# Kernel optimization log

Hardware: AMD Instinct MI355X
Metric: run time of the kernel (lower is better)

Reference implementation:

```python
import jax, jax.numpy as jnp
import numpy as np

DIM = 512
NUM_HEADS = 8
HEAD_DIM = DIM // NUM_HEADS
SCALE = HEAD_DIM ** -0.5


def setup_inputs() -> dict:
    key = jax.random.key(0)
    ks = jax.random.split(key, 11)
    B, T, D = 2, 4096, DIM
    s = 0.02
    return {
        "query": jax.random.normal(ks[0], (B, T, D), jnp.float32),
        "key_": jax.random.normal(ks[1], (B, T, D), jnp.float32),
        "value": jax.random.normal(ks[2], (B, T, D), jnp.float32),
        "Wq": jax.random.normal(ks[3], (D, D), jnp.float32) * s,
        "bq": jnp.zeros((D,), jnp.float32),
        "Wk": jax.random.normal(ks[4], (D, D), jnp.float32) * s,
        "bk": jnp.zeros((D,), jnp.float32),
        "Wv": jax.random.normal(ks[5], (D, D), jnp.float32) * s,
        "bv": jnp.zeros((D,), jnp.float32),
        "Wo": jax.random.normal(ks[6], (D, D), jnp.float32) * s,
        "bo": jnp.zeros((D,), jnp.float32),
    }


def reference(query, key_, value, Wq, bq, Wk, bk, Wv, bv, Wo, bo):
    B, T, D = query.shape
    H, Hd = NUM_HEADS, HEAD_DIM
    # Linear projections (torch Linear: x @ W.T + b)
    q = (query @ Wq.T + bq).reshape(B, T, H, Hd).transpose(0, 2, 1, 3)   # [B,H,T,Hd]
    k = (key_ @ Wk.T + bk).reshape(B, -1, H, Hd).transpose(0, 2, 1, 3)    # [B,H,S,Hd]
    v = (value @ Wv.T + bv).reshape(B, -1, H, Hd).transpose(0, 2, 1, 3)   # [B,H,S,Hd]
    # Full O(T*S) score matrix, as in the original (non-fused) module
    scores = jnp.einsum("bhtd,bhsd->bhts", q, k) * SCALE                  # [B,H,T,S]
    weights = jax.nn.softmax(scores, axis=-1)
    out = jnp.einsum("bhts,bhsd->bhtd", weights, v)                       # [B,H,T,Hd]
    out = out.transpose(0, 2, 1, 3).reshape(B, T, D)
    return out @ Wo.T + bo
```

## Files before the change

### kernel.cpp

```cpp
#include <hip/hip_runtime.h>
#include <cstdint>
#include <cstddef>

typedef __attribute__((ext_vector_type(8))) __bf16 bf16x8;
typedef __attribute__((ext_vector_type(4))) float  f32x4;
typedef __attribute__((ext_vector_type(8))) unsigned short us8;

#define MFMA(a, b, c) __builtin_amdgcn_mfma_f32_16x16x32_bf16((a), (b), (c), 0, 0, 0)

#define QSCALE 0.18033688011112042f

__device__ __forceinline__ unsigned short f2bf(float f) {
  unsigned u = __float_as_uint(f);
  u += 0x7fffu + ((u >> 16) & 1u);
  return (unsigned short)(u >> 16);
}

__device__ __forceinline__ void gload16(const void* g, void* l) {
  __builtin_amdgcn_global_load_lds(
      (__attribute__((address_space(1))) unsigned int*)(uintptr_t)g,
      (__attribute__((address_space(3))) unsigned int*)l,
      16, 0, 0);
}

struct CastArgs {
  const float*    src[7];
  unsigned short* dst[7];
  int             n4[7];
};
__global__ __launch_bounds__(256) void cast_kernel(CastArgs a) {
  int z = blockIdx.y;
  const float* __restrict__ in = a.src[z];
  unsigned short* __restrict__ out = a.dst[z];
  int i = blockIdx.x * 256 + threadIdx.x;
  if (i < a.n4[z]) {
    float4 f = ((const float4*)in)[i];
    ushort4 r;
    r.x = f2bf(f.x); r.y = f2bf(f.y); r.z = f2bf(f.z); r.w = f2bf(f.w);
    ((ushort4*)out)[i] = r;
  }
}

struct ProjArgs {
  const unsigned short* X[3];
  const unsigned short* W[3];
  const float*          bias[3];
  unsigned short*       out[3];
};

__global__ __launch_bounds__(256) void proj_qkv_kernel(ProjArgs args) {
  __shared__ alignas(16) unsigned short smem[64 * 136];
  unsigned short* sA = smem;
  unsigned short* sB = smem + 4096;

  const int z = blockIdx.z;
  const unsigned short* __restrict__ X   = args.X[z];
  const unsigned short* __restrict__ W   = args.W[z];
  const float* __restrict__ bias         = args.bias[z];
  unsigned short* __restrict__ out       = args.out[z];
  const float scl = (z == 0) ? QSCALE : 1.0f;

  const int t = threadIdx.x;
  const int w = t >> 6, lane = t & 63;
  const int quad = lane >> 4, l15 = lane & 15;
  const int wr = w >> 1, wc = w & 1;
  const int m0 = blockIdx.x * 128, n0 = blockIdx.y * 128;

  const int srow = t >> 2;
  const int scol = (((t & 3) ^ (srow & 3)) << 3);

  f32x4 acc[4][4] = {};

  for (int k0 = 0; k0 < 512; k0 += 32) {
    __syncthreads();
    gload16(X + (size_t)(m0 + srow) * 512 + k0 + scol,      &sA[w * 512]);
    gload16(X + (size_t)(m0 + srow + 64) * 512 + k0 + scol, &sA[2048 + w * 512]);
    gload16(W + (size_t)(n0 + srow) * 512 + k0 + scol,      &sB[w * 512]);
    gload16(W + (size_t)(n0 + srow + 64) * 512 + k0 + scol, &sB[2048 + w * 512]);
    asm volatile("s_waitcnt vmcnt(0)" ::: "memory");
    __syncthreads();

    bf16x8 af[4], bfr[4];
#pragma unroll
    for (int mt = 0; mt < 4; ++mt) {
      int ra = wr * 64 + mt * 16 + l15;
      af[mt] = *(const bf16x8*)&sA[ra * 32 + ((quad ^ (ra & 3)) << 3)];
    }
#pragma unroll
    for (int nt = 0; nt < 4; ++nt) {
      int rb = wc * 64 + nt * 16 + l15;
      bfr[nt] = *(const bf16x8*)&sB[rb * 32 + ((quad ^ (rb & 3)) << 3)];
    }
#pragma unroll
    for (int mt = 0; mt < 4; ++mt)
#pragma unroll
      for (int nt = 0; nt < 4; ++nt)
        acc[mt][nt] = MFMA(af[mt], bfr[nt], acc[mt][nt]);
  }

  if (z != 2) {
#pragma unroll
    for (int nt = 0; nt < 4; ++nt) {
      int n = n0 + wc * 64 + nt * 16 + l15;
      float bv = bias[n];
      int h = n >> 6, hd = n & 63;
#pragma unroll
      for (int mt = 0; mt < 4; ++mt) {
#pragma unroll
        for (int r = 0; r < 4; ++r) {
          int m = m0 + wr * 64 + mt * 16 + quad * 4 + r;
          int b = m >> 12, tt = m & 4095;
          out[(((size_t)(b * 8 + h)) * 4096 + tt) * 64 + hd] =
              f2bf((acc[mt][nt][r] + bv) * scl);
        }
      }
    }
  } else {
    const int b   = m0 >> 12;
    const int tt0 = m0 & 4095;
#pragma unroll
    for (int h2 = 0; h2 < 2; ++h2) {
      __syncthreads();
      if (wc == h2) {
#pragma unroll
        for (int nt = 0; nt < 4; ++nt) {
          int nl = nt * 16 + l15;
          float bv = bias[n0 + h2 * 64 + nl];
#pragma unroll
          for (int mt = 0; mt < 4; ++mt)
#pragma unroll
            for (int r = 0; r < 4; ++r) {
              int ml = wr * 64 + mt * 16 + quad * 4 + r;
              smem[nl * 136 + ml] = f2bf((acc[mt][nt][r] + bv) * scl);
            }
        }
      }
      __syncthreads();
      const int row = t >> 2;
      const int c4  = (t & 3) * 8;
      const int n   = n0 + h2 * 64 + row;
      unsigned short* dst = out + ((size_t)(b * 512 + n)) * 4096 + tt0;
#pragma unroll
      for (int k = 0; k < 4; ++k)
        *(us8*)(dst + c4 + k * 32) = *(const us8*)&smem[row * 136 + c4 + k * 32];
    }
  }
}

__global__ __launch_bounds__(256) void proj_out_kernel(
    const unsigned short* __restrict__ X, const unsigned short* __restrict__ W,
    const float* __restrict__ bias, float* __restrict__ out) {
  __shared__ alignas(16) unsigned short sA[128 * 32];
  __shared__ alignas(16) unsigned short sB[128 * 32];

  const int t = threadIdx.x;
  const int w = t >> 6, lane = t & 63;
  const int quad = lane >> 4, l15 = lane & 15;
  const int wr = w >> 1, wc = w & 1;
  const int m0 = blockIdx.x * 128, n0 = blockIdx.y * 128;
  const int srow = t >> 2;
  const int scol = (((t & 3) ^ (srow & 3)) << 3);

  f32x4 acc[4][4] = {};

  for (int k0 = 0; k0 < 512; k0 += 32) {
    __syncthreads();
    gload16(X + (size_t)(m0 + srow) * 512 + k0 + scol,      &sA[w * 512]);
    gload16(X + (size_t)(m0 + srow + 64) * 512 + k0 + scol, &sA[2048 + w * 512]);
    gload16(W + (size_t)(n0 + srow) * 512 + k0 + scol,      &sB[w * 512]);
    gload16(W + (size_t)(n0 + srow + 64) * 512 + k0 + scol, &sB[2048 + w * 512]);
    asm volatile("s_waitcnt vmcnt(0)" ::: "memory");
    __syncthreads();

    bf16x8 af[4], bfr[4];
#pragma unroll
    for (int mt = 0; mt < 4; ++mt) {
      int ra = wr * 64 + mt * 16 + l15;
      af[mt] = *(const bf16x8*)&sA[ra * 32 + ((quad ^ (ra & 3)) << 3)];
    }
#pragma unroll
    for (int nt = 0; nt < 4; ++nt) {
      int rb = wc * 64 + nt * 16 + l15;
      bfr[nt] = *(const bf16x8*)&sB[rb * 32 + ((quad ^ (rb & 3)) << 3)];
    }
#pragma unroll
    for (int mt = 0; mt < 4; ++mt)
#pragma unroll
      for (int nt = 0; nt < 4; ++nt)
        acc[mt][nt] = MFMA(af[mt], bfr[nt], acc[mt][nt]);
  }

#pragma unroll
  for (int nt = 0; nt < 4; ++nt) {
    int n = n0 + wc * 64 + nt * 16 + l15;
    float bv = bias[n];
#pragma unroll
    for (int mt = 0; mt < 4; ++mt) {
#pragma unroll
      for (int r = 0; r < 4; ++r) {
        int m = m0 + wr * 64 + mt * 16 + quad * 4 + r;
        out[(size_t)m * 512 + n] = acc[mt][nt][r] + bv;
      }
    }
  }
}

__global__ __launch_bounds__(256) void attn_kernel(
    const unsigned short* __restrict__ Q, const unsigned short* __restrict__ K,
    const unsigned short* __restrict__ VT, unsigned short* __restrict__ Aout) {
  __shared__ alignas(16) unsigned short kt[64 * 64];
  __shared__ alignas(16) unsigned short vt[64 * 64];
  __shared__ alignas(16) unsigned short pt[4 * 16 * 72];

  const int t = threadIdx.x;
  const int w = t >> 6, lane = t & 63;
  const int quad = lane >> 4, l15 = lane & 15;
  const int bh = blockIdx.y;

  const unsigned short* __restrict__ Qp  = Q  + (size_t)bh * 4096 * 64;
  const unsigned short* __restrict__ Kp  = K  + (size_t)bh * 4096 * 64;
  const unsigned short* __restrict__ VTp = VT + (size_t)bh * 64 * 4096;

  const int q0 = blockIdx.x * 64 + w * 16;

  bf16x8 aq[2];
#pragma unroll
  for (int kk = 0; kk < 2; ++kk)
    aq[kk] = *(const bf16x8*)(Qp + (size_t)(q0 + l15) * 64 + kk * 32 + quad * 8);

  f32x4 o[4] = {};
  float li[4] = {0.f, 0.f, 0.f, 0.f};

  const int grow = t >> 3;
  const int gcol = (((t & 7) ^ (grow & 7)) << 3);

  unsigned short* pw = &pt[w * 16 * 72];

  for (int j = 0; j < 64; ++j) {
    const int s0 = j * 64;
    __syncthreads();
    gload16(Kp + (size_t)(s0 + grow) * 64 + gcol,         &kt[w * 512]);
    gload16(Kp + (size_t)(s0 + grow + 32) * 64 + gcol,    &kt[2048 + w * 512]);
    gload16(VTp + (size_t)grow * 4096 + s0 + gcol,        &vt[w * 512]);
    gload16(VTp + (size_t)(grow + 32) * 4096 + s0 + gcol, &vt[2048 + w * 512]);
    asm volatile("s_waitcnt vmcnt(0)" ::: "memory");
    __syncthreads();

    f32x4 sc[4] = {};
#pragma unroll
    for (int nt = 0; nt < 4; ++nt) {
#pragma unroll
      for (int kk = 0; kk < 2; ++kk) {
        bf16x8 kf = *(const bf16x8*)&kt[(nt * 16 + l15) * 64 +
                                        (((kk * 4 + quad) ^ (l15 & 7)) << 3)];
        sc[nt] = MFMA(aq[kk], kf, sc[nt]);
      }
    }

#pragma unroll
    for (int nt = 0; nt < 4; ++nt) {
#pragma unroll
      for (int r = 0; r < 4; ++r) {
        float p = __builtin_amdgcn_exp2f(sc[nt][r]);
        li[r] += p;
        pw[(quad * 4 + r) * 72 + nt * 16 + l15] = f2bf(p);
      }
    }

    asm volatile("s_waitcnt lgkmcnt(0)" ::: "memory");

    bf16x8 pa[2];
#pragma unroll
    for (int kk = 0; kk < 2; ++kk)
      pa[kk] = *(const bf16x8*)&pw[l15 * 72 + kk * 32 + quad * 8];

#pragma unroll
    for (int nt = 0; nt < 4; ++nt) {
#pragma unroll
      for (int kk = 0; kk < 2; ++kk) {
        bf16x8 vf = *(const bf16x8*)&vt[(nt * 16 + l15) * 64 +
                                        (((kk * 4 + quad) ^ (l15 & 7)) << 3)];
        o[nt] = MFMA(pa[kk], vf, o[nt]);
      }
    }
  }

#pragma unroll
  for (int r = 0; r < 4; ++r) {
    float s = li[r];
    s += __shfl_xor(s, 1, 64);
    s += __shfl_xor(s, 2, 64);
    s += __shfl_xor(s, 4, 64);
    s += __shfl_xor(s, 8, 64);
    li[r] = s;
  }

  const int b = bh >> 3, h = bh & 7;
#pragma unroll
  for (int nt = 0; nt < 4; ++nt) {
#pragma unroll
    for (int r = 0; r < 4; ++r) {
      int tt = q0 + quad * 4 + r;
      float val = o[nt][r] / li[r];
      Aout[((size_t)b * 4096 + tt) * 512 + h * 64 + nt * 16 + l15] = f2bf(val);
    }
  }
}

extern "C" void kernel_launch(void* const* d_in, const int* in_sizes, int n_in,
                              void* d_out, int out_size, void* d_ws, size_t ws_size,
                              hipStream_t stream) {
  (void)in_sizes; (void)n_in; (void)out_size; (void)ws_size;
  const float* query = (const float*)d_in[0];
  const float* key_  = (const float*)d_in[1];
  const float* value = (const float*)d_in[2];
  const float* Wq = (const float*)d_in[3];
  const float* bq = (const float*)d_in[4];
  const float* Wk = (const float*)d_in[5];
  const float* bk = (const float*)d_in[6];
  const float* Wv = (const float*)d_in[7];
  const float* bv = (const float*)d_in[8];
  const float* Wo = (const float*)d_in[9];
  const float* bo = (const float*)d_in[10];
  float* out = (float*)d_out;

  char* ws = (char*)d_ws;
  const size_t MB = 1024 * 1024;
  unsigned short* Xq  = (unsigned short*)(ws + 0 * MB);
  unsigned short* Xk  = (unsigned short*)(ws + 8 * MB);
  unsigned short* Xv  = (unsigned short*)(ws + 16 * MB);
  unsigned short* Wqb = (unsigned short*)(ws + 24 * MB);
  unsigned short* Wkb = (unsigned short*)(ws + 24 * MB + 512 * 1024);
  unsigned short* Wvb = (unsigned short*)(ws + 25 * MB);
  unsigned short* Wob = (unsigned short*)(ws + 25 * MB + 512 * 1024);
  unsigned short* qb  = (unsigned short*)(ws + 26 * MB);
  unsigned short* kb  = (unsigned short*)(ws + 34 * MB);
  unsigned short* vtb = (unsigned short*)(ws + 42 * MB);
  unsigned short* ao  = Xq;

  CastArgs ca;
  ca.src[0] = query; ca.src[1] = key_; ca.src[2] = value;
  ca.src[3] = Wq;    ca.src[4] = Wk;   ca.src[5] = Wv;  ca.src[6] = Wo;
  ca.dst[0] = Xq;    ca.dst[1] = Xk;   ca.dst[2] = Xv;
  ca.dst[3] = Wqb;   ca.dst[4] = Wkb;  ca.dst[5] = Wvb; ca.dst[6] = Wob;
  ca.n4[0] = ca.n4[1] = ca.n4[2] = 1048576;
  ca.n4[3] = ca.n4[4] = ca.n4[5] = ca.n4[6] = 65536;
  cast_kernel<<<dim3(4096, 7), 256, 0, stream>>>(ca);

  ProjArgs pa;
  pa.X[0] = Xq;  pa.X[1] = Xk;  pa.X[2] = Xv;
  pa.W[0] = Wqb; pa.W[1] = Wkb; pa.W[2] = Wvb;
  pa.bias[0] = bq; pa.bias[1] = bk; pa.bias[2] = bv;
  pa.out[0] = qb; pa.out[1] = kb; pa.out[2] = vtb;
  proj_qkv_kernel<<<dim3(64, 4, 3), 256, 0, stream>>>(pa);

  attn_kernel<<<dim3(64, 16), 256, 0, stream>>>(qb, kb, vtb, ao);

  proj_out_kernel<<<dim3(64, 4), 256, 0, stream>>>(ao, Wob, bo, out);
}
```

Baseline: 267.1 us.

## Double-buffer GEMM and attention loads, switch attention to 32x32 MFMA register softmax

Both projection GEMMs now double-buffer their LDS tiles, prefetching the next K slice while MFMAs run on the current one. The attention kernel is restructured: each wave handles 32 query rows using 32x32x16 MFMAs computing S^T, and K/V tiles are double-buffered. Probabilities stay in registers, packed to bf16 and exchanged across lanes with shuffles, which removes the LDS round-trip for P. The grid is halved, workgroup indices are swizzled for L2 locality, and launch bounds request two blocks per CU. The risks are higher register pressure and the correctness of the lane/row mapping in the new shuffle-based P layout.

After: 240.5 us. 1.11x faster.

```diff
diff --git a/kernel.cpp b/kernel.cpp
--- a/kernel.cpp
+++ b/kernel.cpp
@@ -2,11 +2,13 @@
 #include <cstdint>
 #include <cstddef>
 
-typedef __attribute__((ext_vector_type(8))) __bf16 bf16x8;
-typedef __attribute__((ext_vector_type(4))) float  f32x4;
-typedef __attribute__((ext_vector_type(8))) unsigned short us8;
-
-#define MFMA(a, b, c) __builtin_amdgcn_mfma_f32_16x16x32_bf16((a), (b), (c), 0, 0, 0)
+typedef __attribute__((ext_vector_type(8)))  __bf16 bf16x8;
+typedef __attribute__((ext_vector_type(4)))  float  f32x4;
+typedef __attribute__((ext_vector_type(16))) float  f32x16;
+typedef __attribute__((ext_vector_type(8)))  unsigned short us8;
+
+#define MFMA(a, b, c)   __builtin_amdgcn_mfma_f32_16x16x32_bf16((a), (b), (c), 0, 0, 0)
+#define MFMA32(a, b, c) __builtin_amdgcn_mfma_f32_32x32x16_bf16((a), (b), (c), 0, 0, 0)
 
 #define QSCALE 0.18033688011112042f
 
@@ -14,6 +16,12 @@
   unsigned u = __float_as_uint(f);
   u += 0x7fffu + ((u >> 16) & 1u);
   return (unsigned short)(u >> 16);
+}
+
+__device__ __forceinline__ unsigned pk2bf(float lo, float hi) {
+  unsigned a = __float_as_uint(lo) + 0x8000u;
+  unsigned b = __float_as_uint(hi) + 0x8000u;
+  return __builtin_amdgcn_perm(b, a, 0x07060302u);
 }
 
 __device__ __forceinline__ void gload16(const void* g, void* l) {
@@ -49,9 +57,7 @@
 };
 
 __global__ __launch_bounds__(256) void proj_qkv_kernel(ProjArgs args) {
-  __shared__ alignas(16) unsigned short smem[64 * 136];
-  unsigned short* sA = smem;
-  unsigned short* sB = smem + 4096;
+  __shared__ alignas(16) unsigned short smem[16384];
 
   const int z = blockIdx.z;
   const unsigned short* __restrict__ X   = args.X[z];
@@ -71,14 +77,33 @@
 
   f32x4 acc[4][4] = {};
 
+  {
+    unsigned short* sA = smem;
+    unsigned short* sB = smem + 4096;
+    gload16(X + (size_t)(m0 + srow) * 512 + scol,      &sA[w * 512]);
+    gload16(X + (size_t)(m0 + srow + 64) * 512 + scol, &sA[2048 + w * 512]);
+    gload16(W + (size_t)(n0 + srow) * 512 + scol,      &sB[w * 512]);
+    gload16(W + (size_t)(n0 + srow + 64) * 512 + scol, &sB[2048 + w * 512]);
+  }
+
   for (int k0 = 0; k0 < 512; k0 += 32) {
-    __syncthreads();
-    gload16(X + (size_t)(m0 + srow) * 512 + k0 + scol,      &sA[w * 512]);
-    gload16(X + (size_t)(m0 + srow + 64) * 512 + k0 + scol, &sA[2048 + w * 512]);
-    gload16(W + (size_t)(n0 + srow) * 512 + k0 + scol,      &sB[w * 512]);
-    gload16(W + (size_t)(n0 + srow + 64) * 512 + k0 + scol, &sB[2048 + w * 512]);
-    asm volatile("s_waitcnt vmcnt(0)" ::: "memory");
-    __syncthreads();
+    const int buf = (k0 >> 5) & 1;
+    unsigned short* sA = smem + buf * 8192;
+    unsigned short* sB = sA + 4096;
+    if (k0 < 480) {
+      unsigned short* nA = smem + (buf ^ 1) * 8192;
+      unsigned short* nB = nA + 4096;
+      const int kn = k0 + 32;
+      gload16(X + (size_t)(m0 + srow) * 512 + kn + scol,      &nA[w * 512]);
+      gload16(X + (size_t)(m0 + srow + 64) * 512 + kn + scol, &nA[2048 + w * 512]);
+      gload16(W + (size_t)(n0 + srow) * 512 + kn + scol,      &nB[w * 512]);
+      gload16(W + (size_t)(n0 + srow + 64) * 512 + kn + scol, &nB[2048 + w * 512]);
+      asm volatile("s_waitcnt vmcnt(4)" ::: "memory");
+    } else {
+      asm volatile("s_waitcnt vmcnt(0)" ::: "memory");
+    }
+    __builtin_amdgcn_s_barrier();
+    asm volatile("" ::: "memory");
 
     bf16x8 af[4], bfr[4];
 #pragma unroll
@@ -96,6 +121,9 @@
 #pragma unroll
       for (int nt = 0; nt < 4; ++nt)
         acc[mt][nt] = MFMA(af[mt], bfr[nt], acc[mt][nt]);
+
+    asm volatile("" ::: "memory");
+    __builtin_amdgcn_s_barrier();
   }
 
   if (z != 2) {
@@ -150,8 +178,7 @@
 __global__ __launch_bounds__(256) void proj_out_kernel(
     const unsigned short* __restrict__ X, const unsigned short* __restrict__ W,
     const float* __restrict__ bias, float* __restrict__ out) {
-  __shared__ alignas(16) unsigned short sA[128 * 32];
-  __shared__ alignas(16) unsigned short sB[128 * 32];
+  __shared__ alignas(16) unsigned short smem[16384];
 
   const int t = threadIdx.x;
   const int w = t >> 6, lane = t & 63;
@@ -163,14 +190,33 @@
 
   f32x4 acc[4][4] = {};
 
+  {
+    unsigned short* sA = smem;
+    unsigned short* sB = smem + 4096;
+    gload16(X + (size_t)(m0 + srow) * 512 + scol,      &sA[w * 512]);
+    gload16(X + (size_t)(m0 + srow + 64) * 512 + scol, &sA[2048 + w * 512]);
+    gload16(W + (size_t)(n0 + srow) * 512 + scol,      &sB[w * 512]);
+    gload16(W + (size_t)(n0 + srow + 64) * 512 + scol, &sB[2048 + w * 512]);
+  }
+
   for (int k0 = 0; k0 < 512; k0 += 32) {
-    __syncthreads();
-    gload16(X + (size_t)(m0 + srow) * 512 + k0 + scol,      &sA[w * 512]);
-    gload16(X + (size_t)(m0 + srow + 64) * 512 + k0 + scol, &sA[2048 + w * 512]);
-    gload16(W + (size_t)(n0 + srow) * 512 + k0 + scol,      &sB[w * 512]);
-    gload16(W + (size_t)(n0 + srow + 64) * 512 + k0 + scol, &sB[2048 + w * 512]);
-    asm volatile("s_waitcnt vmcnt(0)" ::: "memory");
-    __syncthreads();
+    const int buf = (k0 >> 5) & 1;
+    unsigned short* sA = smem + buf * 8192;
+    unsigned short* sB = sA + 4096;
+    if (k0 < 480) {
+      unsigned short* nA = smem + (buf ^ 1) * 8192;
+      unsigned short* nB = nA + 4096;
+      const int kn = k0 + 32;
+      gload16(X + (size_t)(m0 + srow) * 512 + kn + scol,      &nA[w * 512]);
+      gload16(X + (size_t)(m0 + srow + 64) * 512 + kn + scol, &nA[2048 + w * 512]);
+      gload16(W + (size_t)(n0 + srow) * 512 + kn + scol,      &nB[w * 512]);
+      gload16(W + (size_t)(n0 + srow + 64) * 512 + kn + scol, &nB[2048 + w * 512]);
+      asm volatile("s_waitcnt vmcnt(4)" ::: "memory");
+    } else {
+      asm volatile("s_waitcnt vmcnt(0)" ::: "memory");
+    }
+    __builtin_amdgcn_s_barrier();
+    asm volatile("" ::: "memory");
 
     bf16x8 af[4], bfr[4];
 #pragma unroll
@@ -188,6 +234,9 @@
 #pragma unroll
       for (int nt = 0; nt < 4; ++nt)
         acc[mt][nt] = MFMA(af[mt], bfr[nt], acc[mt][nt]);
+
+    asm volatile("" ::: "memory");
+    __builtin_amdgcn_s_barrier();
   }
 
 #pragma unroll
@@ -205,105 +254,128 @@
   }
 }
 
-__global__ __launch_bounds__(256) void attn_kernel(
+__global__ __launch_bounds__(256, 2) void attn_kernel(
     const unsigned short* __restrict__ Q, const unsigned short* __restrict__ K,
     const unsigned short* __restrict__ VT, unsigned short* __restrict__ Aout) {
-  __shared__ alignas(16) unsigned short kt[64 * 64];
-  __shared__ alignas(16) unsigned short vt[64 * 64];
-  __shared__ alignas(16) unsigned short pt[4 * 16 * 72];
+  __shared__ alignas(16) unsigned short kt[2][4096];
+  __shared__ alignas(16) unsigned short vt[2][4096];
+  __shared__ float lis[128];
 
   const int t = threadIdx.x;
   const int w = t >> 6, lane = t & 63;
-  const int quad = lane >> 4, l15 = lane & 15;
-  const int bh = blockIdx.y;
+  const int l31 = lane & 31, h = lane >> 5;
+
+  const int wg  = blockIdx.x + gridDim.x * blockIdx.y;
+  const int swz = (wg & 7) * 64 + (wg >> 3);
+  const int bx = swz & 31, bh = swz >> 5;
 
   const unsigned short* __restrict__ Qp  = Q  + (size_t)bh * 4096 * 64;
   const unsigned short* __restrict__ Kp  = K  + (size_t)bh * 4096 * 64;
   const unsigned short* __restrict__ VTp = VT + (size_t)bh * 64 * 4096;
 
-  const int q0 = blockIdx.x * 64 + w * 16;
-
-  bf16x8 aq[2];
-#pragma unroll
-  for (int kk = 0; kk < 2; ++kk)
-    aq[kk] = *(const bf16x8*)(Qp + (size_t)(q0 + l15) * 64 + kk * 32 + quad * 8);
-
-  f32x4 o[4] = {};
-  float li[4] = {0.f, 0.f, 0.f, 0.f};
+  const int q0w = bx * 128 + w * 32;
 
   const int grow = t >> 3;
   const int gcol = (((t & 7) ^ (grow & 7)) << 3);
 
-  unsigned short* pw = &pt[w * 16 * 72];
+  {
+    gload16(Kp + (size_t)grow * 64 + gcol,               &kt[0][w * 512]);
+    gload16(Kp + (size_t)(grow + 32) * 64 + gcol,        &kt[0][2048 + w * 512]);
+    gload16(VTp + (size_t)grow * 4096 + gcol,            &vt[0][w * 512]);
+    gload16(VTp + (size_t)(grow + 32) * 4096 + gcol,     &vt[0][2048 + w * 512]);
+  }
+
+  bf16x8 aq[4];
+#pragma unroll
+  for (int kd = 0; kd < 4; ++kd)
+    aq[kd] = *(const bf16x8*)(Qp + (size_t)(q0w + l31) * 64 + kd * 16 + h * 8);
+
+  f32x16 o0 = {}, o1 = {};
+  float li = 0.f;
+
+  const int swzk = (l31 & 7) << 3;
+  const int rA0 = l31 * 64, rA1 = (l31 + 32) * 64;
 
   for (int j = 0; j < 64; ++j) {
-    const int s0 = j * 64;
-    __syncthreads();
-    gload16(Kp + (size_t)(s0 + grow) * 64 + gcol,         &kt[w * 512]);
-    gload16(Kp + (size_t)(s0 + grow + 32) * 64 + gcol,    &kt[2048 + w * 512]);
-    gload16(VTp + (size_t)grow * 4096 + s0 + gcol,        &vt[w * 512]);
-    gload16(VTp + (size_t)(grow + 32) * 4096 + s0 + gcol, &vt[2048 + w * 512]);
-    asm volatile("s_waitcnt vmcnt(0)" ::: "memory");
-    __syncthreads();
-
-    f32x4 sc[4] = {};
-#pragma unroll
-    for (int nt = 0; nt < 4; ++nt) {
-#pragma unroll
-      for (int kk = 0; kk < 2; ++kk) {
-        bf16x8 kf = *(const bf16x8*)&kt[(nt * 16 + l15) * 64 +
-                                        (((kk * 4 + quad) ^ (l15 & 7)) << 3)];
-        sc[nt] = MFMA(aq[kk], kf, sc[nt]);
-      }
-    }
-
-#pragma unroll
-    for (int nt = 0; nt < 4; ++nt) {
-#pragma unroll
-      for (int r = 0; r < 4; ++r) {
-        float p = __builtin_amdgcn_exp2f(sc[nt][r]);
-        li[r] += p;
-        pw[(quad * 4 + r) * 72 + nt * 16 + l15] = f2bf(p);
-      }
-    }
-
-    asm volatile("s_waitcnt lgkmcnt(0)" ::: "memory");
-
-    bf16x8 pa[2];
-#pragma unroll
-    for (int kk = 0; kk < 2; ++kk)
-      pa[kk] = *(const bf16x8*)&pw[l15 * 72 + kk * 32 + quad * 8];
-
-#pragma unroll
-    for (int nt = 0; nt < 4; ++nt) {
-#pragma unroll
-      for (int kk = 0; kk < 2; ++kk) {
-        bf16x8 vf = *(const bf16x8*)&vt[(nt * 16 + l15) * 64 +
-                                        (((kk * 4 + quad) ^ (l15 & 7)) << 3)];
-        o[nt] = MFMA(pa[kk], vf, o[nt]);
-      }
-    }
-  }
-
-#pragma unroll
-  for (int r = 0; r < 4; ++r) {
-    float s = li[r];
-    s += __shfl_xor(s, 1, 64);
-    s += __shfl_xor(s, 2, 64);
-    s += __shfl_xor(s, 4, 64);
-    s += __shfl_xor(s, 8, 64);
-    li[r] = s;
-  }
-
-  const int b = bh >> 3, h = bh & 7;
-#pragma unroll
-  for (int nt = 0; nt < 4; ++nt) {
-#pragma unroll
-    for (int r = 0; r < 4; ++r) {
-      int tt = q0 + quad * 4 + r;
-      float val = o[nt][r] / li[r];
-      Aout[((size_t)b * 4096 + tt) * 512 + h * 64 + nt * 16 + l15] = f2bf(val);
-    }
+    const int cb = j & 1, nb = cb ^ 1;
+    if (j < 63) {
+      const int s0 = (j + 1) * 64;
+      gload16(Kp + (size_t)(s0 + grow) * 64 + gcol,          &kt[nb][w * 512]);
+      gload16(Kp + (size_t)(s0 + grow + 32) * 64 + gcol,     &kt[nb][2048 + w * 512]);
+      gload16(VTp + (size_t)grow * 4096 + s0 + gcol,         &vt[nb][w * 512]);
+      gload16(VTp + (size_t)(grow + 32) * 4096 + s0 + gcol,  &vt[nb][2048 + w * 512]);
+      asm volatile("s_waitcnt vmcnt(4)" ::: "memory");
+    } else {
+      asm volatile("s_waitcnt vmcnt(0)" ::: "memory");
+    }
+    __builtin_amdgcn_s_barrier();
+    asm volatile("" ::: "memory");
+
+    const unsigned short* ktb = kt[cb];
+    const unsigned short* vtb = vt[cb];
+
+    f32x16 scv0 = {}, scv1 = {};
+#pragma unroll
+    for (int kd = 0; kd < 4; ++kd) {
+      bf16x8 k0 = *(const bf16x8*)&ktb[rA0 + ((((2 * kd + h) << 3) ^ swzk))];
+      bf16x8 k1 = *(const bf16x8*)&ktb[rA1 + ((((2 * kd + h) << 3) ^ swzk))];
+      scv0 = MFMA32(k0, aq[kd], scv0);
+      scv1 = MFMA32(k1, aq[kd], scv1);
+    }
+
+    float p0[16], p1[16];
+#pragma unroll
+    for (int r = 0; r < 16; ++r) {
+      p0[r] = __builtin_amdgcn_exp2f(scv0[r]);
+      p1[r] = __builtin_amdgcn_exp2f(scv1[r]);
+      li += p0[r] + p1[r];
+    }
+
+    unsigned Xg[8], Yg[8];
+#pragma unroll
+    for (int g = 0; g < 8; ++g) {
+      const float* pp = (g < 4) ? p0 : p1;
+      const int b4 = (g & 3) * 4;
+      Xg[g] = pk2bf(pp[b4 + 0], pp[b4 + 1]);
+      Yg[g] = pk2bf(pp[b4 + 2], pp[b4 + 3]);
+    }
+
+#pragma unroll
+    for (int ks = 0; ks < 4; ++ks) {
+      unsigned Lx = h ? Xg[2 * ks + 1] : Xg[2 * ks];
+      unsigned Mx = h ? Xg[2 * ks]     : Xg[2 * ks + 1];
+      unsigned Ly = h ? Yg[2 * ks + 1] : Yg[2 * ks];
+      unsigned My = h ? Yg[2 * ks]     : Yg[2 * ks + 1];
+      unsigned sMx = (unsigned)__shfl_xor((int)Mx, 32, 64);
+      unsigned sMy = (unsigned)__shfl_xor((int)My, 32, 64);
+      union { unsigned u[4]; bf16x8 v; } pa;
+      pa.u[0] = h ? sMx : Lx;
+      pa.u[1] = h ? sMy : Ly;
+      pa.u[2] = h ? Lx  : sMx;
+      pa.u[3] = h ? Ly  : sMy;
+      bf16x8 v0 = *(const bf16x8*)&vtb[rA0 + ((((2 * ks + h) << 3) ^ swzk))];
+      bf16x8 v1 = *(const bf16x8*)&vtb[rA1 + ((((2 * ks + h) << 3) ^ swzk))];
+      o0 = MFMA32(pa.v, v0, o0);
+      o1 = MFMA32(pa.v, v1, o1);
+    }
+
+    asm volatile("" ::: "memory");
+    __builtin_amdgcn_s_barrier();
+  }
+
+  li += __shfl_xor(li, 32);
+  if (h == 0) lis[w * 32 + l31] = li;
+  __syncthreads();
+
+  const int bq = bh >> 3, hh = bh & 7;
+#pragma unroll
+  for (int r = 0; r < 16; ++r) {
+    const int qloc = (r & 3) + 8 * (r >> 2) + 4 * h;
+    const float inv = 1.0f / lis[w * 32 + qloc];
+    const int trow = q0w + qloc;
+    const size_t base = ((size_t)bq * 4096 + trow) * 512 + hh * 64;
+    Aout[base + l31]      = f2bf(o0[r] * inv);
+    Aout[base + 32 + l31] = f2bf(o1[r] * inv);
   }
 }
 
@@ -354,7 +426,7 @@
   pa.out[0] = qb; pa.out[1] = kb; pa.out[2] = vtb;
   proj_qkv_kernel<<<dim3(64, 4, 3), 256, 0, stream>>>(pa);
 
-  attn_kernel<<<dim3(64, 16), 256, 0, stream>>>(qb, kb, vtb, ao);
+  attn_kernel<<<dim3(32, 16), 256, 0, stream>>>(qb, kb, vtb, ao);
 
   proj_out_kernel<<<dim3(64, 4), 256, 0, stream>>>(ao, Wob, bo, out);
 }
```
